# Kernel optimization log

Measured on AMD Instinct MI355X. Metric: run time of the kernel, lower is better.

The kernel has to match this reference:

```python
import jax, jax.numpy as jnp
import numpy as np

EPS = 1e-8


def _conv1d(x, w, b):
    # x: [B, E, L], w: [F, E, K], b: [F] -> [B, F, L] (k=3, pad=1 keeps length)
    y = jax.lax.conv_general_dilated(
        x, w, window_strides=(1,), padding=[(1, 1)],
        dimension_numbers=("NCH", "OIH", "NCH"))
    return y + b[None, :, None]


def setup_inputs() -> dict:
    key = jax.random.key(0)
    kq, ka, ke, kw, kb, ku = jax.random.split(key, 6)
    B, QL, AL = 512, 128, 512
    V, E, F, K = 50000, 300, 400, 3
    question = jax.random.randint(kq, (B, QL), 0, V + 1, dtype=jnp.int64)
    answer = jax.random.randint(ka, (B, AL), 0, V + 1, dtype=jnp.int64)
    emb_table = jax.random.normal(ke, (V + 1, E), dtype=jnp.float32)
    emb_table = emb_table.at[0].set(0.0)  # padding_idx=0
    conv_w = jax.random.normal(kw, (F, E, K), dtype=jnp.float32) * 0.05
    conv_b = jax.random.normal(kb, (F,), dtype=jnp.float32) * 0.05
    U = jax.random.normal(ku, (F, F), dtype=jnp.float32) * 0.1
    return {"question": question, "answer": answer, "emb_table": emb_table,
            "conv_w": conv_w, "conv_b": conv_b, "U": U}


def reference(question, answer, emb_table, conv_w, conv_b, U):
    q = emb_table[question]              # [B, QL, E]
    a = emb_table[answer]                # [B, AL, E]
    Q = _conv1d(q.transpose(0, 2, 1), conv_w, conv_b)   # [B, F, QL]
    A = _conv1d(a.transpose(0, 2, 1), conv_w, conv_b)   # [B, F, AL]
    # G = tanh(Q^T U A): [B, QL, AL]
    G = jnp.tanh(jnp.einsum("bfq,fg,bga->bqa", Q, U, A))
    roQ = jax.nn.softmax(jnp.max(G, axis=2), axis=1)    # [B, QL]
    roA = jax.nn.softmax(jnp.max(G, axis=1), axis=1)    # [B, AL]
    rQ = jnp.einsum("bfq,bq->bf", Q, roQ)               # [B, F]
    rA = jnp.einsum("bfa,ba->bf", A, roA)               # [B, F]
    nQ = jnp.maximum(jnp.linalg.norm(rQ, axis=1), EPS)
    nA = jnp.maximum(jnp.linalg.norm(rA, axis=1), EPS)
    return jnp.sum(rQ * rA, axis=1) / (nQ * nA)         # [B]
```

## Files before the change

kernel.cpp:

```cpp
#include <hip/hip_runtime.h>
#include <math.h>

typedef unsigned int   uint32;
typedef unsigned short ushort16;
typedef __attribute__((ext_vector_type(8))) short  short8;
typedef __attribute__((ext_vector_type(4))) float  floatx4;

#define Bb   512
#define QLn  128
#define ALn  512
#define En   300
#define Fn   400
#define OW   416
#define EPAD 320
#define NV   50001
#define ECROWS 50176
#define ECSTRIDE 2560

typedef const __attribute__((address_space(1))) unsigned int guint_t;
typedef __attribute__((address_space(3))) unsigned int luint_t;
#define GLDS16(g, l) __builtin_amdgcn_global_load_lds((guint_t*)(g), (luint_t*)(l), 16, 0, 0)

static __device__ __forceinline__ float bf_lo(uint32 u) { return __uint_as_float(u << 16); }
static __device__ __forceinline__ float bf_hi(uint32 u) { return __uint_as_float(u & 0xffff0000u); }
static __device__ __forceinline__ ushort16 f2bf(float f) {
    uint32 u = __float_as_uint(f);
    uint32 r = (u + 0x7fffu + ((u >> 16) & 1u)) >> 16;
    return (ushort16)r;
}
static __device__ __forceinline__ uint32 pack2(float a, float b) {
    return (uint32)f2bf(a) | ((uint32)f2bf(b) << 16);
}

__global__ __launch_bounds__(128) void embcvt_kernel(
        const float* __restrict__ emb, char* __restrict__ embbf)
{
    const int r = blockIdx.x, j = threadIdx.x;
    const float* er = emb + (size_t)r * En;
    uint32* orow = (uint32*)(embbf + (size_t)r * 640);
    for (int d = j; d < 160; d += 128) {
        uint32 v = 0;
        if (d < 150) {
            float2 f2v = *(const float2*)(er + 2 * d);
            v = pack2(f2v.x, f2v.y);
        }
        orow[d] = v;
    }
}

__global__ __launch_bounds__(256) void prep_wt(
        const float* __restrict__ W, const float* __restrict__ cb,
        ushort16* __restrict__ Wt2, float* __restrict__ bias2)
{
    const int f = blockIdx.x, t = threadIdx.x;
    for (int p2 = t; p2 < 480; p2 += 256) {
        int p = 2 * p2;
        float v0 = 0.f, v1 = 0.f;
        if (f < Fn) {
            int kk = p / EPAD, e = p - kk * EPAD;
            if (e < En)     v0 = W[(size_t)f * 900 + e * 3 + kk];
            if (e + 1 < En) v1 = W[(size_t)f * 900 + (e + 1) * 3 + kk];
        }
        *(uint32*)&Wt2[(size_t)f * 960 + p] = pack2(v0, v1);
    }
    if (t == 0) bias2[f] = (f < Fn) ? cb[f] : 0.f;
}

__global__ __launch_bounds__(256) void prep_ub(
        const float* __restrict__ U, ushort16* __restrict__ Ub)
{
    const int g = blockIdx.x, t = threadIdx.x;
    uint32* orow = (uint32*)(Ub + (size_t)g * 416);
    for (int f2 = t; f2 < 208; f2 += 256) {
        int f = 2 * f2;
        float v0 = 0.f, v1 = 0.f;
        if (g < Fn) {
            if (f < Fn)     v0 = U[(size_t)f * Fn + g];
            if (f + 1 < Fn) v1 = U[(size_t)(f + 1) * Fn + g];
        }
        orow[f2] = pack2(v0, v1);
    }
}

__global__ __launch_bounds__(512) void ec_gemm(
        const char* __restrict__ embbf, const char* __restrict__ Wt2,
        char* __restrict__ EC)
{
    __shared__ __align__(16) char As[32768];
    __shared__ __align__(16) char Bs[32768];
    const int t = threadIdx.x, lane = t & 63, w = t >> 6;
    const int v0 = blockIdx.x * 256, c0 = blockIdx.y * 256;
    const int wr = w >> 2, wc = w & 3;
    const int fm = lane & 15;
    const int cg = ((lane & 3) - ((lane >> 3) & 3)) & 3;
    const int rl = lane >> 2;
    const int chunkOff = (((lane >> 4) + (fm >> 1)) & 3) * 16;

    const char* srcA[2];
    const char* srcB[2];
#pragma unroll
    for (int i = 0; i < 2; ++i) {
        srcA[i] = embbf + (size_t)(v0 + w * 32 + i * 16 + rl) * 640 + cg * 16;
        int n = c0 + w * 32 + i * 16 + rl;
        int kk = n / 416, f = n - kk * 416;
        if (n >= 1248) { kk = 0; f = 508; }
        srcB[i] = Wt2 + (size_t)f * 1920 + kk * 640 + cg * 16;
    }
    char* AsW = As + w * 2048;
    char* BsW = Bs + w * 2048;

    floatx4 acc[8][4];
    const floatx4 zz = {0.f, 0.f, 0.f, 0.f};
#pragma unroll
    for (int m = 0; m < 8; ++m)
#pragma unroll
        for (int n = 0; n < 4; ++n) acc[m][n] = zz;

#define ESTG(ko, buf) do {                                                    \
        const int _ko = (ko); const int _bo = (buf) * 16384;                  \
        GLDS16(srcA[0] + _ko, AsW + _bo);                                     \
        GLDS16(srcA[1] + _ko, AsW + _bo + 1024);                              \
        GLDS16(srcB[0] + _ko, BsW + _bo);                                     \
        GLDS16(srcB[1] + _ko, BsW + _bo + 1024);                              \
    } while (0)

    int cur = 0;
    ESTG(0, 0);
    __syncthreads();
    for (int ks = 0; ks < 10; ++ks) {
        const int nxt = cur ^ 1;
        if (ks < 9) ESTG((ks + 1) * 64, nxt);
        short8 af[8], bfv[4];
        const char* Ac = As + cur * 16384;
        const char* Bc = Bs + cur * 16384;
#pragma unroll
        for (int m = 0; m < 8; ++m)
            af[m] = *(const short8*)(Ac + (wr * 128 + m * 16 + fm) * 64 + chunkOff);
#pragma unroll
        for (int n = 0; n < 4; ++n)
            bfv[n] = *(const short8*)(Bc + (wc * 64 + n * 16 + fm) * 64 + chunkOff);
        __builtin_amdgcn_s_setprio(1);
#pragma unroll
        for (int m = 0; m < 8; ++m)
#pragma unroll
            for (int n = 0; n < 4; ++n)
                acc[m][n] = __builtin_amdgcn_mfma_f32_16x16x32_bf16(
                    af[m], bfv[n], acc[m][n], 0, 0, 0);
        __builtin_amdgcn_s_setprio(0);
        __syncthreads();
        cur = nxt;
    }
#undef ESTG

#pragma unroll
    for (int m = 0; m < 8; ++m) {
        const int v = v0 + wr * 128 + m * 16 + ((lane >> 4) * 4);
#pragma unroll
        for (int n = 0; n < 4; ++n) {
            const int col = c0 + wc * 64 + n * 16 + fm;
#pragma unroll
            for (int r = 0; r < 4; ++r)
                *(ushort16*)(EC + (size_t)(v + r) * ECSTRIDE + col * 2) =
                    f2bf(acc[m][n][r]);
        }
    }
}

__global__ __launch_bounds__(256) void gather_conv(
        const int* __restrict__ toks, const char* __restrict__ EC,
        const float* __restrict__ bias2, char* __restrict__ outb,
        int nb, int L)
{
    const int total = nb * L * 52;
    int id = blockIdx.x * 256 + threadIdx.x;
    const int stride = gridDim.x * 256;
    for (; id < total; id += stride) {
        const uint32 uid = (uint32)id;
        const int c = (int)(uid % 52u);
        const int r = (int)(uid / 52u);
        const int l = r & (L - 1), b = r / L;
        const int* tr = toks + (size_t)b * L;
        const int t0 = (l > 0)     ? tr[l - 1] : 0;
        const int t1 = tr[l];
        const int t2 = (l < L - 1) ? tr[l + 1] : 0;
        const uint4 x0 = *(const uint4*)(EC + (size_t)t0 * ECSTRIDE +        c * 16);
        const uint4 x1 = *(const uint4*)(EC + (size_t)t1 * ECSTRIDE +  832 + c * 16);
        const uint4 x2 = *(const uint4*)(EC + (size_t)t2 * ECSTRIDE + 1664 + c * 16);
        const float4 b0 = *(const float4*)(bias2 + c * 8);
        const float4 b1 = *(const float4*)(bias2 + c * 8 + 4);
        uint4 o;
        o.x = pack2(bf_lo(x0.x) + bf_lo(x1.x) + bf_lo(x2.x) + b0.x,
                    bf_hi(x0.x) + bf_hi(x1.x) + bf_hi(x2.x) + b0.y);
        o.y = pack2(bf_lo(x0.y) + bf_lo(x1.y) + bf_lo(x2.y) + b0.z,
                    bf_hi(x0.y) + bf_hi(x1.y) + bf_hi(x2.y) + b0.w);
        o.z = pack2(bf_lo(x0.z) + bf_lo(x1.z) + bf_lo(x2.z) + b1.x,
                    bf_hi(x0.z) + bf_hi(x1.z) + bf_hi(x2.z) + b1.y);
        o.w = pack2(bf_lo(x0.w) + bf_lo(x1.w) + bf_lo(x2.w) + b1.z,
                    bf_hi(x0.w) + bf_hi(x1.w) + bf_hi(x2.w) + b1.w);
        *(uint4*)(outb + (size_t)r * 832 + c * 16) = o;
    }
}

template<int NWM, int NWN, int MF, int NF, int BR>
static __device__ __forceinline__ void qp_tile(
        const char* __restrict__ Qb, const char* __restrict__ Ub,
        char* __restrict__ ob, int col0, char* As, char* Bs)
{
    const int t = threadIdx.x, lane = t & 63, w = t >> 6;
    const int wr = w / NWN, wc = w % NWN;
    const int fm = lane & 15;
    const int cg = ((lane & 3) - ((lane >> 3) & 3)) & 3;
    const int rl = lane >> 2;
    const int chunkOff = (((lane >> 4) + (fm >> 1)) & 3) * 16;

    const char* srcA = Qb + (size_t)(w * 16 + rl) * 832 + cg * 16;
    const char* srcB0; const char* srcB1 = 0;
    if (BR == 256) {
        srcB0 = Ub + (size_t)(col0 + w * 32 + rl) * 832 + cg * 16;
        srcB1 = srcB0 + (size_t)16 * 832;
    } else {
        srcB0 = Ub + (size_t)(col0 + w * 16 + rl) * 832 + cg * 16;
        srcB1 = Ub + (size_t)(col0 + 128 + w * 16 + rl) * 832 + cg * 16;
    }
    char* AsW = As + w * 1024;
    char* BsW0; char* BsW1;
    if (BR == 256) { BsW0 = Bs + w * 2048; BsW1 = BsW0 + 1024; }
    else           { BsW0 = Bs + w * 1024; BsW1 = Bs + 8192 + w * 1024; }
    const int BUFB = BR * 64;

    floatx4 acc[MF][NF];
    const floatx4 zz = {0.f, 0.f, 0.f, 0.f};
#pragma unroll
    for (int m = 0; m < MF; ++m)
#pragma unroll
        for (int n = 0; n < NF; ++n) acc[m][n] = zz;

#define QSTG(ko, buf) do {                                                    \
        const int _ko = (ko);                                                 \
        GLDS16(srcA + _ko, AsW + (buf) * 8192);                               \
        GLDS16(srcB0 + _ko, BsW0 + (buf) * BUFB);                             \
        if (BR == 256 || w < 2) GLDS16(srcB1 + _ko, BsW1 + (buf) * BUFB);     \
    } while (0)

    int cur = 0;
    QSTG(0, 0);
    __syncthreads();
    for (int ks = 0; ks < 13; ++ks) {
        const int nxt = cur ^ 1;
        if (ks < 12) QSTG((ks + 1) * 64, nxt);
        short8 af[MF], bfv[NF];
        const char* Ac = As + cur * 8192;
        const char* Bc = Bs + cur * BUFB;
#pragma unroll
        for (int m = 0; m < MF; ++m)
            af[m] = *(const short8*)(Ac + (wr * (MF * 16) + m * 16 + fm) * 64 + chunkOff);
#pragma unroll
        for (int n = 0; n < NF; ++n)
            bfv[n] = *(const short8*)(Bc + (wc * (NF * 16) + n * 16 + fm) * 64 + chunkOff);
        __builtin_amdgcn_s_setprio(1);
#pragma unroll
        for (int m = 0; m < MF; ++m)
#pragma unroll
            for (int n = 0; n < NF; ++n)
                acc[m][n] = __builtin_amdgcn_mfma_f32_16x16x32_bf16(
                    af[m], bfv[n], acc[m][n], 0, 0, 0);
        __builtin_amdgcn_s_setprio(0);
        __syncthreads();
        cur = nxt;
    }
#undef QSTG

#pragma unroll
    for (int m = 0; m < MF; ++m) {
        const int row = wr * (MF * 16) + m * 16 + ((lane >> 4) * 4);
#pragma unroll
        for (int n = 0; n < NF; ++n) {
            const int col = col0 + wc * (NF * 16) + n * 16 + fm;
#pragma unroll
            for (int r = 0; r < 4; ++r)
                *(ushort16*)(ob + (size_t)(row + r) * 832 + col * 2) =
                    f2bf(acc[m][n][r]);
        }
    }
}

__global__ __launch_bounds__(512) void qp_gemm(
        const char* __restrict__ qb, const char* __restrict__ Ub,
        char* __restrict__ qpb)
{
    __shared__ __align__(16) char As[16384];
    __shared__ __align__(16) char Bs[32768];
    const int bx = blockIdx.x;
    const int b = bx >> 1, nt = bx & 1;
    const char* Qb = qb + (size_t)b * 106496;
    char* ob = qpb + (size_t)b * 106496;
    if (nt == 0)
        qp_tile<2, 4, 4, 4, 256>(Qb, Ub, ob, 0, As, Bs);
    else
        qp_tile<4, 2, 2, 5, 160>(Qb, Ub, ob, 256, As, Bs);
}

__global__ __launch_bounds__(256) void fused_g(
        const ushort16* __restrict__ Qp,
        const ushort16* __restrict__ Av,
        float* __restrict__ rowPart,
        float* __restrict__ colMg,
        int nb)
{
    __shared__ __align__(16) char Qs[16384];
    __shared__ __align__(16) char Asl[16384];
    __shared__ float rowM2[128][2];
    __shared__ float colM2[128][2];

    const int t = threadIdx.x, lane = t & 63, w = t >> 6;
    const int bx = blockIdx.x;
    const int xcd = bx & 7, rest = bx >> 3;
    const int c = rest & 3, g = rest >> 2;
    const int T = g * 8 + xcd;
    if (T >= nb) return;
    const int b = T;
    const int wr = w >> 1, wc = w & 1;
    const int fm = lane & 15;
    const int cg = ((lane & 3) - ((lane >> 3) & 3)) & 3;
    const int srow = w * 16 + (lane >> 2);
    const int chunkOff = (((lane >> 4) + (fm >> 1)) & 3) * 16;

    const char* Qpb = (const char*)Qp + (size_t)b * 106496;
    const char* Ab  = (const char*)Av + (size_t)b * 425984 + (size_t)c * 106496;
    const char* srcQ = Qpb + (size_t)srow * 832 + cg * 16;
    const char* srcA = Ab  + (size_t)srow * 832 + cg * 16;
    char* QsW = Qs + w * 1024;
    char* AsW = Asl + w * 1024;

    floatx4 acc[4][4];
    const floatx4 zz = {0.f, 0.f, 0.f, 0.f};
#pragma unroll
    for (int m = 0; m < 4; ++m)
#pragma unroll
        for (int n = 0; n < 4; ++n) acc[m][n] = zz;

#define GSTAGE(colb, buf) do {                                                \
        const int _c = (colb); const int _o = (buf) * 8192;                   \
        GLDS16(srcQ + _c,         QsW + _o);                                  \
        GLDS16(srcQ + 53248 + _c, QsW + _o + 4096);                           \
        GLDS16(srcA + _c,         AsW + _o);                                  \
        GLDS16(srcA + 53248 + _c, AsW + _o + 4096);                           \
    } while (0)

    int cur = 0;
    GSTAGE(0, 0);
    __syncthreads();

    for (int ks = 0; ks < 13; ++ks) {
        const int nxt = cur ^ 1;
        if (ks < 12) GSTAGE((ks + 1) * 64, nxt);

        short8 qa[4], aa_[4];
        const char* Qc = Qs + cur * 8192;
        const char* Ac = Asl + cur * 8192;
#pragma unroll
        for (int m = 0; m < 4; ++m)
            qa[m] = *(const short8*)(Qc + (wr * 64 + m * 16 + fm) * 64 + chunkOff);
#pragma unroll
        for (int n = 0; n < 4; ++n)
            aa_[n] = *(const short8*)(Ac + (wc * 64 + n * 16 + fm) * 64 + chunkOff);
        __builtin_amdgcn_s_setprio(1);
#pragma unroll
        for (int m = 0; m < 4; ++m)
#pragma unroll
            for (int n = 0; n < 4; ++n)
                acc[m][n] = __builtin_amdgcn_mfma_f32_16x16x32_bf16(
                    qa[m], aa_[n], acc[m][n], 0, 0, 0);
        __builtin_amdgcn_s_setprio(0);
        __syncthreads();
        cur = nxt;
    }
#undef GSTAGE

#pragma unroll
    for (int m = 0; m < 4; ++m)
#pragma unroll
        for (int r = 0; r < 4; ++r) {
            float v = fmaxf(fmaxf(acc[m][0][r], acc[m][1][r]),
                            fmaxf(acc[m][2][r], acc[m][3][r]));
            v = fmaxf(v, __shfl_xor(v, 1));
            v = fmaxf(v, __shfl_xor(v, 2));
            v = fmaxf(v, __shfl_xor(v, 4));
            v = fmaxf(v, __shfl_xor(v, 8));
            if (fm == 0) rowM2[wr * 64 + m * 16 + (lane >> 4) * 4 + r][wc] = v;
        }
#pragma unroll
    for (int n = 0; n < 4; ++n) {
        float v = -1e30f;
#pragma unroll
        for (int m = 0; m < 4; ++m)
#pragma unroll
            for (int r = 0; r < 4; ++r) v = fmaxf(v, acc[m][n][r]);
        v = fmaxf(v, __shfl_xor(v, 16));
        v = fmaxf(v, __shfl_xor(v, 32));
        if (lane < 16) colM2[wc * 64 + n * 16 + lane][wr] = v;
    }
    __syncthreads();
    if (t < 128) {
        rowPart[((size_t)b * 4 + c) * 128 + t] = fmaxf(rowM2[t][0], rowM2[t][1]);
        colMg[(size_t)b * 512 + c * 128 + t]   = fmaxf(colM2[t][0], colM2[t][1]);
    }
}

static __device__ __forceinline__ float block_reduce_max(float v, volatile float* red) {
    int t = threadIdx.x;
    red[t] = v; __syncthreads();
    for (int s = 128; s > 0; s >>= 1) {
        if (t < s) red[t] = fmaxf(red[t], red[t + s]);
        __syncthreads();
    }
    float r = red[0]; __syncthreads();
    return r;
}
static __device__ __forceinline__ float block_reduce_sum(float v, volatile float* red) {
    int t = threadIdx.x;
    red[t] = v; __syncthreads();
    for (int s = 128; s > 0; s >>= 1) {
        if (t < s) red[t] = red[t] + red[t + s];
        __syncthreads();
    }
    float r = red[0]; __syncthreads();
    return r;
}

__global__ __launch_bounds__(256) void fused_pool(
        const ushort16* __restrict__ Qv,
        const ushort16* __restrict__ Av,
        const float* __restrict__ rowPart,
        const float* __restrict__ colMg,
        float* __restrict__ out)
{
    __shared__ float colv[ALn];
    __shared__ float roq[QLn];
    __shared__ float red[256];
    const int t = threadIdx.x, b = blockIdx.x;

    float v = -1e30f;
    if (t < QLn) {
        const float* rp = rowPart + (size_t)b * 512;
        float rm = fmaxf(fmaxf(rp[t], rp[128 + t]), fmaxf(rp[256 + t], rp[384 + t]));
        v = tanhf(rm);
    }
    float vmax = block_reduce_max(v, red);
    float ex = (t < QLn) ? __expf(v - vmax) : 0.f;
    float ssum = block_reduce_sum(ex, red);
    if (t < QLn) roq[t] = ex / ssum;

    float c0 = tanhf(colMg[(size_t)b * 512 + t]);
    float c1 = tanhf(colMg[(size_t)b * 512 + 256 + t]);
    float cmax = block_reduce_max(fmaxf(c0, c1), red);
    float e0 = __expf(c0 - cmax), e1 = __expf(c1 - cmax);
    float csum = block_reduce_sum(e0 + e1, red);
    colv[t] = e0 / csum;
    colv[t + 256] = e1 / csum;
    __syncthreads();

    float rq0 = 0.f, rq1 = 0.f, ra0 = 0.f, ra1 = 0.f;
    if (t < 208) {
        const uint32* Qb32 = (const uint32*)((const char*)Qv + (size_t)b * 106496);
#pragma unroll 4
        for (int q = 0; q < QLn; ++q) {
            float wv = roq[q];
            uint32 u = Qb32[q * 208 + t];
            rq0 = fmaf(bf_lo(u), wv, rq0);
            rq1 = fmaf(bf_hi(u), wv, rq1);
        }
        const uint32* Ab32 = (const uint32*)((const char*)Av + (size_t)b * 425984);
#pragma unroll 4
        for (int a = 0; a < ALn; ++a) {
            float wv = colv[a];
            uint32 u = Ab32[a * 208 + t];
            ra0 = fmaf(bf_lo(u), wv, ra0);
            ra1 = fmaf(bf_hi(u), wv, ra1);
        }
    }

    float dd  = block_reduce_sum(rq0 * ra0 + rq1 * ra1, red);
    float qq  = block_reduce_sum(rq0 * rq0 + rq1 * rq1, red);
    float aam = block_reduce_sum(ra0 * ra0 + ra1 * ra1, red);
    if (t == 0) {
        float nq = fmaxf(sqrtf(qq), 1e-8f);
        float na = fmaxf(sqrtf(aam), 1e-8f);
        out[b] = dd / (nq * na);
    }
}

extern "C" void kernel_launch(void* const* d_in, const int* in_sizes, int n_in,
                              void* d_out, int out_size, void* d_ws, size_t ws_size,
                              hipStream_t stream)
{
    const int*   question = (const int*)d_in[0];
    const int*   answer   = (const int*)d_in[1];
    const float* emb      = (const float*)d_in[2];
    const float* conv_w   = (const float*)d_in[3];
    const float* conv_b   = (const float*)d_in[4];
    const float* U        = (const float*)d_in[5];
    float* out = (float*)d_out;
    char* ws = (char*)d_ws;

    const size_t WT2B   = (size_t)512 * 960 * 2;
    const size_t UBB    = (size_t)416 * 416 * 2;
    const size_t ECB    = (size_t)ECROWS * ECSTRIDE;
    const size_t FIXED0 = WT2B + 2048 + UBB + ECB;
    const size_t QB     = (size_t)QLn * OW * 2;
    const size_t AB     = (size_t)ALn * OW * 2;
    const size_t MXB    = 4096;
    const size_t PER_B  = 2 * QB + AB + MXB;

    size_t avail = (ws_size > FIXED0) ? (ws_size - FIXED0) : 0;
    int CB = (int)(avail / PER_B);
    if (CB > Bb) CB = Bb;
    if (CB < 1)  CB = 1;
    int nch = (Bb + CB - 1) / CB;
    int CBe = (Bb + nch - 1) / nch;

    char*  wt2   = ws;
    float* bias2 = (float*)(ws + WT2B);
    char*  ub    = ws + WT2B + 2048;
    char*  EC    = ws + WT2B + 2048 + UBB;
    char*  embbf = ws + FIXED0;
    char*  qb    = ws + FIXED0;
    char*  qpb   = qb  + (size_t)CB * QB;
    char*  ab    = qpb + (size_t)CB * QB;
    float* rowP  = (float*)(ab + (size_t)CB * AB);
    float* colM  = rowP + (size_t)CB * 512;

    embcvt_kernel<<<NV, 128, 0, stream>>>(emb, embbf);
    prep_wt<<<512, 256, 0, stream>>>(conv_w, conv_b, (ushort16*)wt2, bias2);
    prep_ub<<<416, 256, 0, stream>>>(U, (ushort16*)ub);
    ec_gemm<<<dim3(196, 5), 512, 0, stream>>>(embbf, wt2, EC);

    for (int b0 = 0; b0 < Bb; b0 += CBe) {
        int nb = (Bb - b0 < CBe) ? (Bb - b0) : CBe;
        gather_conv<<<1024, 256, 0, stream>>>(
            question + (size_t)b0 * QLn, EC, bias2, qb, nb, QLn);
        gather_conv<<<4096, 256, 0, stream>>>(
            answer + (size_t)b0 * ALn, EC, bias2, ab, nb, ALn);
        qp_gemm<<<nb * 2, 512, 0, stream>>>(qb, ub, qpb);

        int blocksG = ((nb + 7) / 8) * 8 * 4;
        fused_g<<<blocksG, 256, 0, stream>>>((const ushort16*)qpb, (const ushort16*)ab,
                                             rowP, colM, nb);
        fused_pool<<<nb, 256, 0, stream>>>((const ushort16*)qb, (const ushort16*)ab,
                                           rowP, colM, out + b0);
    }
}
```

Baseline: 668.2 us.

## Retile EC GEMM, merge gather kernels, and enlarge fused_g tiles

ec_gemm now keeps a 128-row slab of embeddings resident in LDS across all five output column chunks and streams only the weight tiles, so the A operand is loaded once per block instead of once per column block. The two gather_conv launches become a single gather_both launch to save one launch per batch chunk. fused_g now covers 256 answer columns per block with the full 128 Q rows (two blocks per batch row instead of four), writes column maxima straight to global memory, and halves the rowPart partials. The larger LDS footprint (112KB in ec_gemm) and larger accumulator tiles may reduce occupancy, and the XCD-aware block ordering in fused_g is dropped.

```diff
diff --git a/kernel.cpp b/kernel.cpp
--- a/kernel.cpp
+++ b/kernel.cpp
@@ -86,118 +86,140 @@
         const char* __restrict__ embbf, const char* __restrict__ Wt2,
         char* __restrict__ EC)
 {
-    __shared__ __align__(16) char As[32768];
+    __shared__ __align__(16) char As[81920];
     __shared__ __align__(16) char Bs[32768];
     const int t = threadIdx.x, lane = t & 63, w = t >> 6;
-    const int v0 = blockIdx.x * 256, c0 = blockIdx.y * 256;
+    const int v0 = blockIdx.x * 128;
     const int wr = w >> 2, wc = w & 3;
     const int fm = lane & 15;
     const int cg = ((lane & 3) - ((lane >> 3) & 3)) & 3;
     const int rl = lane >> 2;
     const int chunkOff = (((lane >> 4) + (fm >> 1)) & 3) * 16;
 
-    const char* srcA[2];
-    const char* srcB[2];
-#pragma unroll
-    for (int i = 0; i < 2; ++i) {
-        srcA[i] = embbf + (size_t)(v0 + w * 32 + i * 16 + rl) * 640 + cg * 16;
-        int n = c0 + w * 32 + i * 16 + rl;
-        int kk = n / 416, f = n - kk * 416;
-        if (n >= 1248) { kk = 0; f = 508; }
-        srcB[i] = Wt2 + (size_t)f * 1920 + kk * 640 + cg * 16;
-    }
-    char* AsW = As + w * 2048;
-    char* BsW = Bs + w * 2048;
-
-    floatx4 acc[8][4];
-    const floatx4 zz = {0.f, 0.f, 0.f, 0.f};
-#pragma unroll
-    for (int m = 0; m < 8; ++m)
-#pragma unroll
-        for (int n = 0; n < 4; ++n) acc[m][n] = zz;
-
-#define ESTG(ko, buf) do {                                                    \
-        const int _ko = (ko); const int _bo = (buf) * 16384;                  \
-        GLDS16(srcA[0] + _ko, AsW + _bo);                                     \
-        GLDS16(srcA[1] + _ko, AsW + _bo + 1024);                              \
-        GLDS16(srcB[0] + _ko, BsW + _bo);                                     \
-        GLDS16(srcB[1] + _ko, BsW + _bo + 1024);                              \
+    uint32 offB[5][2];
+#pragma unroll
+    for (int c = 0; c < 5; ++c)
+#pragma unroll
+        for (int i = 0; i < 2; ++i) {
+            int n = c * 256 + w * 32 + i * 16 + rl;
+            int kk = n / 416, f = n - kk * 416;
+            if (n >= 1248) { kk = 0; f = 508; }
+            offB[c][i] = (uint32)(f * 1920 + kk * 640 + cg * 16);
+        }
+
+    const char* srcA = embbf + (size_t)(v0 + w * 16 + rl) * 640 + cg * 16;
+#pragma unroll
+    for (int ks = 0; ks < 10; ++ks)
+        GLDS16(srcA + ks * 64, As + ks * 8192 + w * 1024);
+
+#define BSTG(c, ks, buf) do {                                                 \
+        GLDS16(Wt2 + offB[c][0] + (ks) * 64,                                  \
+               Bs + (buf) * 16384 + w * 2048);                                \
+        GLDS16(Wt2 + offB[c][1] + (ks) * 64,                                  \
+               Bs + (buf) * 16384 + w * 2048 + 1024);                         \
     } while (0)
 
     int cur = 0;
-    ESTG(0, 0);
+    BSTG(0, 0, 0);
     __syncthreads();
-    for (int ks = 0; ks < 10; ++ks) {
-        const int nxt = cur ^ 1;
-        if (ks < 9) ESTG((ks + 1) * 64, nxt);
-        short8 af[8], bfv[4];
-        const char* Ac = As + cur * 16384;
-        const char* Bc = Bs + cur * 16384;
-#pragma unroll
-        for (int m = 0; m < 8; ++m)
-            af[m] = *(const short8*)(Ac + (wr * 128 + m * 16 + fm) * 64 + chunkOff);
-#pragma unroll
-        for (int n = 0; n < 4; ++n)
-            bfv[n] = *(const short8*)(Bc + (wc * 64 + n * 16 + fm) * 64 + chunkOff);
-        __builtin_amdgcn_s_setprio(1);
-#pragma unroll
-        for (int m = 0; m < 8; ++m)
+
+#pragma unroll
+    for (int c = 0; c < 5; ++c) {
+        floatx4 acc[4][4];
+        const floatx4 zz = {0.f, 0.f, 0.f, 0.f};
+#pragma unroll
+        for (int m = 0; m < 4; ++m)
+#pragma unroll
+            for (int n = 0; n < 4; ++n) acc[m][n] = zz;
+
+        for (int ks = 0; ks < 10; ++ks) {
+            const int nxt = cur ^ 1;
+            if (ks < 9)      BSTG(c, ks + 1, nxt);
+            else if (c < 4)  BSTG(c + 1, 0, nxt);
+
+            short8 af[4], bfv[4];
+            const char* Ak = As + ks * 8192;
+            const char* Bc = Bs + cur * 16384;
+#pragma unroll
+            for (int m = 0; m < 4; ++m)
+                af[m] = *(const short8*)(Ak + (wr * 64 + m * 16 + fm) * 64 + chunkOff);
 #pragma unroll
             for (int n = 0; n < 4; ++n)
-                acc[m][n] = __builtin_amdgcn_mfma_f32_16x16x32_bf16(
-                    af[m], bfv[n], acc[m][n], 0, 0, 0);
-        __builtin_amdgcn_s_setprio(0);
-        __syncthreads();
-        cur = nxt;
-    }
-#undef ESTG
-
-#pragma unroll
-    for (int m = 0; m < 8; ++m) {
-        const int v = v0 + wr * 128 + m * 16 + ((lane >> 4) * 4);
-#pragma unroll
-        for (int n = 0; n < 4; ++n) {
-            const int col = c0 + wc * 64 + n * 16 + fm;
-#pragma unroll
-            for (int r = 0; r < 4; ++r)
-                *(ushort16*)(EC + (size_t)(v + r) * ECSTRIDE + col * 2) =
-                    f2bf(acc[m][n][r]);
-        }
-    }
-}
-
-__global__ __launch_bounds__(256) void gather_conv(
+                bfv[n] = *(const short8*)(Bc + (wc * 64 + n * 16 + fm) * 64 + chunkOff);
+            __builtin_amdgcn_s_setprio(1);
+#pragma unroll
+            for (int m = 0; m < 4; ++m)
+#pragma unroll
+                for (int n = 0; n < 4; ++n)
+                    acc[m][n] = __builtin_amdgcn_mfma_f32_16x16x32_bf16(
+                        af[m], bfv[n], acc[m][n], 0, 0, 0);
+            __builtin_amdgcn_s_setprio(0);
+            __syncthreads();
+            cur = nxt;
+        }
+
+#pragma unroll
+        for (int m = 0; m < 4; ++m) {
+            const int v = v0 + wr * 64 + m * 16 + ((lane >> 4) * 4);
+#pragma unroll
+            for (int n = 0; n < 4; ++n) {
+                const int col = c * 256 + wc * 64 + n * 16 + fm;
+#pragma unroll
+                for (int r = 0; r < 4; ++r)
+                    *(ushort16*)(EC + (size_t)(v + r) * ECSTRIDE + col * 2) =
+                        f2bf(acc[m][n][r]);
+            }
+        }
+    }
+#undef BSTG
+}
+
+static __device__ __forceinline__ void gather_one(
         const int* __restrict__ toks, const char* __restrict__ EC,
         const float* __restrict__ bias2, char* __restrict__ outb,
-        int nb, int L)
-{
-    const int total = nb * L * 52;
-    int id = blockIdx.x * 256 + threadIdx.x;
-    const int stride = gridDim.x * 256;
-    for (; id < total; id += stride) {
-        const uint32 uid = (uint32)id;
-        const int c = (int)(uid % 52u);
-        const int r = (int)(uid / 52u);
-        const int l = r & (L - 1), b = r / L;
-        const int* tr = toks + (size_t)b * L;
-        const int t0 = (l > 0)     ? tr[l - 1] : 0;
-        const int t1 = tr[l];
-        const int t2 = (l < L - 1) ? tr[l + 1] : 0;
-        const uint4 x0 = *(const uint4*)(EC + (size_t)t0 * ECSTRIDE +        c * 16);
-        const uint4 x1 = *(const uint4*)(EC + (size_t)t1 * ECSTRIDE +  832 + c * 16);
-        const uint4 x2 = *(const uint4*)(EC + (size_t)t2 * ECSTRIDE + 1664 + c * 16);
-        const float4 b0 = *(const float4*)(bias2 + c * 8);
-        const float4 b1 = *(const float4*)(bias2 + c * 8 + 4);
-        uint4 o;
-        o.x = pack2(bf_lo(x0.x) + bf_lo(x1.x) + bf_lo(x2.x) + b0.x,
-                    bf_hi(x0.x) + bf_hi(x1.x) + bf_hi(x2.x) + b0.y);
-        o.y = pack2(bf_lo(x0.y) + bf_lo(x1.y) + bf_lo(x2.y) + b0.z,
-                    bf_hi(x0.y) + bf_hi(x1.y) + bf_hi(x2.y) + b0.w);
-        o.z = pack2(bf_lo(x0.z) + bf_lo(x1.z) + bf_lo(x2.z) + b1.x,
-                    bf_hi(x0.z) + bf_hi(x1.z) + bf_hi(x2.z) + b1.y);
-        o.w = pack2(bf_lo(x0.w) + bf_lo(x1.w) + bf_lo(x2.w) + b1.z,
-                    bf_hi(x0.w) + bf_hi(x1.w) + bf_hi(x2.w) + b1.w);
-        *(uint4*)(outb + (size_t)r * 832 + c * 16) = o;
+        int id, int L)
+{
+    const uint32 uid = (uint32)id;
+    const int c = (int)(uid % 52u);
+    const int r = (int)(uid / 52u);
+    const int l = r & (L - 1), b = r / L;
+    const int* tr = toks + (size_t)b * L;
+    const int t0 = (l > 0)     ? tr[l - 1] : 0;
+    const int t1 = tr[l];
+    const int t2 = (l < L - 1) ? tr[l + 1] : 0;
+    const uint4 x0 = *(const uint4*)(EC + (size_t)t0 * ECSTRIDE +        c * 16);
+    const uint4 x1 = *(const uint4*)(EC + (size_t)t1 * ECSTRIDE +  832 + c * 16);
+    const uint4 x2 = *(const uint4*)(EC + (size_t)t2 * ECSTRIDE + 1664 + c * 16);
+    const float4 b0 = *(const float4*)(bias2 + c * 8);
+    const float4 b1 = *(const float4*)(bias2 + c * 8 + 4);
+    uint4 o;
+    o.x = pack2(bf_lo(x0.x) + bf_lo(x1.x) + bf_lo(x2.x) + b0.x,
+                bf_hi(x0.x) + bf_hi(x1.x) + bf_hi(x2.x) + b0.y);
+    o.y = pack2(bf_lo(x0.y) + bf_lo(x1.y) + bf_lo(x2.y) + b0.z,
+                bf_hi(x0.y) + bf_hi(x1.y) + bf_hi(x2.y) + b0.w);
+    o.z = pack2(bf_lo(x0.z) + bf_lo(x1.z) + bf_lo(x2.z) + b1.x,
+                bf_hi(x0.z) + bf_hi(x1.z) + bf_hi(x2.z) + b1.y);
+    o.w = pack2(bf_lo(x0.w) + bf_lo(x1.w) + bf_lo(x2.w) + b1.z,
+                bf_hi(x0.w) + bf_hi(x1.w) + bf_hi(x2.w) + b1.w);
+    *(uint4*)(outb + (size_t)r * 832 + c * 16) = o;
+}
+
+#define GQB 1024
+#define GAB 4096
+__global__ __launch_bounds__(256) void gather_both(
+        const int* __restrict__ question, const int* __restrict__ answer,
+        const char* __restrict__ EC, const float* __restrict__ bias2,
+        char* __restrict__ qb, char* __restrict__ ab, int nb)
+{
+    const int bx = blockIdx.x, t = threadIdx.x;
+    if (bx < GQB) {
+        const int total = nb * QLn * 52;
+        for (int id = bx * 256 + t; id < total; id += GQB * 256)
+            gather_one(question, EC, bias2, qb, id, QLn);
+    } else {
+        const int total = nb * ALn * 52;
+        for (int id = (bx - GQB) * 256 + t; id < total; id += GAB * 256)
+            gather_one(answer, EC, bias2, ab, id, ALn);
     }
 }
 
@@ -308,65 +330,61 @@
         int nb)
 {
     __shared__ __align__(16) char Qs[16384];
-    __shared__ __align__(16) char Asl[16384];
-    __shared__ float rowM2[128][2];
-    __shared__ float colM2[128][2];
+    __shared__ __align__(16) char Asl[32768];
+    __shared__ float rowM4[128][4];
 
     const int t = threadIdx.x, lane = t & 63, w = t >> 6;
     const int bx = blockIdx.x;
-    const int xcd = bx & 7, rest = bx >> 3;
-    const int c = rest & 3, g = rest >> 2;
-    const int T = g * 8 + xcd;
-    if (T >= nb) return;
-    const int b = T;
-    const int wr = w >> 1, wc = w & 1;
+    const int c = bx & 1, b = bx >> 1;
+    if (b >= nb) return;
     const int fm = lane & 15;
     const int cg = ((lane & 3) - ((lane >> 3) & 3)) & 3;
-    const int srow = w * 16 + (lane >> 2);
+    const int rl = lane >> 2;
     const int chunkOff = (((lane >> 4) + (fm >> 1)) & 3) * 16;
 
     const char* Qpb = (const char*)Qp + (size_t)b * 106496;
-    const char* Ab  = (const char*)Av + (size_t)b * 425984 + (size_t)c * 106496;
-    const char* srcQ = Qpb + (size_t)srow * 832 + cg * 16;
-    const char* srcA = Ab  + (size_t)srow * 832 + cg * 16;
-    char* QsW = Qs + w * 1024;
-    char* AsW = Asl + w * 1024;
-
-    floatx4 acc[4][4];
+    const char* Ab  = (const char*)Av + (size_t)b * 425984 + (size_t)c * 212992;
+    const char* srcQ0 = Qpb + (size_t)(w * 16 + rl) * 832 + cg * 16;
+    const char* srcQ1 = Qpb + (size_t)(64 + w * 16 + rl) * 832 + cg * 16;
+    const char* srcA0 = Ab  + (size_t)(w * 64 + rl) * 832 + cg * 16;
+
+    floatx4 acc[8][4];
     const floatx4 zz = {0.f, 0.f, 0.f, 0.f};
 #pragma unroll
-    for (int m = 0; m < 4; ++m)
+    for (int m = 0; m < 8; ++m)
 #pragma unroll
         for (int n = 0; n < 4; ++n) acc[m][n] = zz;
 
-#define GSTAGE(colb, buf) do {                                                \
-        const int _c = (colb); const int _o = (buf) * 8192;                   \
-        GLDS16(srcQ + _c,         QsW + _o);                                  \
-        GLDS16(srcQ + 53248 + _c, QsW + _o + 4096);                           \
-        GLDS16(srcA + _c,         AsW + _o);                                  \
-        GLDS16(srcA + 53248 + _c, AsW + _o + 4096);                           \
+#define FSTG(ko, buf) do {                                                    \
+        const int _ko = (ko);                                                 \
+        GLDS16(srcQ0 + _ko, Qs + (buf) * 8192 + w * 1024);                    \
+        GLDS16(srcQ1 + _ko, Qs + (buf) * 8192 + 4096 + w * 1024);             \
+        GLDS16(srcA0 + _ko,         Asl + (buf) * 16384 + w * 4096);          \
+        GLDS16(srcA0 + 13312 + _ko, Asl + (buf) * 16384 + w * 4096 + 1024);   \
+        GLDS16(srcA0 + 26624 + _ko, Asl + (buf) * 16384 + w * 4096 + 2048);   \
+        GLDS16(srcA0 + 39936 + _ko, Asl + (buf) * 16384 + w * 4096 + 3072);   \
     } while (0)
 
     int cur = 0;
-    GSTAGE(0, 0);
+    FSTG(0, 0);
     __syncthreads();
 
     for (int ks = 0; ks < 13; ++ks) {
         const int nxt = cur ^ 1;
-        if (ks < 12) GSTAGE((ks + 1) * 64, nxt);
-
-        short8 qa[4], aa_[4];
+        if (ks < 12) FSTG((ks + 1) * 64, nxt);
+
+        short8 qa[8], aa_[4];
         const char* Qc = Qs + cur * 8192;
-        const char* Ac = Asl + cur * 8192;
-#pragma unroll
-        for (int m = 0; m < 4; ++m)
-            qa[m] = *(const short8*)(Qc + (wr * 64 + m * 16 + fm) * 64 + chunkOff);
+        const char* Ac = Asl + cur * 16384;
+#pragma unroll
+        for (int m = 0; m < 8; ++m)
+            qa[m] = *(const short8*)(Qc + (m * 16 + fm) * 64 + chunkOff);
 #pragma unroll
         for (int n = 0; n < 4; ++n)
-            aa_[n] = *(const short8*)(Ac + (wc * 64 + n * 16 + fm) * 64 + chunkOff);
+            aa_[n] = *(const short8*)(Ac + (w * 64 + n * 16 + fm) * 64 + chunkOff);
         __builtin_amdgcn_s_setprio(1);
 #pragma unroll
-        for (int m = 0; m < 4; ++m)
+        for (int m = 0; m < 8; ++m)
 #pragma unroll
             for (int n = 0; n < 4; ++n)
                 acc[m][n] = __builtin_amdgcn_mfma_f32_16x16x32_bf16(
@@ -375,10 +393,10 @@
         __syncthreads();
         cur = nxt;
     }
-#undef GSTAGE
-
-#pragma unroll
-    for (int m = 0; m < 4; ++m)
+#undef FSTG
+
+#pragma unroll
+    for (int m = 0; m < 8; ++m)
 #pragma unroll
         for (int r = 0; r < 4; ++r) {
             float v = fmaxf(fmaxf(acc[m][0][r], acc[m][1][r]),
@@ -387,24 +405,25 @@
             v = fmaxf(v, __shfl_xor(v, 2));
             v = fmaxf(v, __shfl_xor(v, 4));
             v = fmaxf(v, __shfl_xor(v, 8));
-            if (fm == 0) rowM2[wr * 64 + m * 16 + (lane >> 4) * 4 + r][wc] = v;
+            if (fm == 0) rowM4[m * 16 + (lane >> 4) * 4 + r][w] = v;
         }
 #pragma unroll
     for (int n = 0; n < 4; ++n) {
         float v = -1e30f;
 #pragma unroll
-        for (int m = 0; m < 4; ++m)
+        for (int m = 0; m < 8; ++m)
 #pragma unroll
             for (int r = 0; r < 4; ++r) v = fmaxf(v, acc[m][n][r]);
         v = fmaxf(v, __shfl_xor(v, 16));
         v = fmaxf(v, __shfl_xor(v, 32));
-        if (lane < 16) colM2[wc * 64 + n * 16 + lane][wr] = v;
+        if (lane < 16)
+            colMg[(size_t)b * 512 + c * 256 + w * 64 + n * 16 + lane] = v;
     }
     __syncthreads();
-    if (t < 128) {
-        rowPart[((size_t)b * 4 + c) * 128 + t] = fmaxf(rowM2[t][0], rowM2[t][1]);
-        colMg[(size_t)b * 512 + c * 128 + t]   = fmaxf(colM2[t][0], colM2[t][1]);
-    }
+    if (t < 128)
+        rowPart[((size_t)b * 2 + c) * 128 + t] =
+            fmaxf(fmaxf(rowM4[t][0], rowM4[t][1]),
+                  fmaxf(rowM4[t][2], rowM4[t][3]));
 }
 
 static __device__ __forceinline__ float block_reduce_max(float v, volatile float* red) {
@@ -442,8 +461,8 @@
 
     float v = -1e30f;
     if (t < QLn) {
-        const float* rp = rowPart + (size_t)b * 512;
-        float rm = fmaxf(fmaxf(rp[t], rp[128 + t]), fmaxf(rp[256 + t], rp[384 + t]));
+        const float* rp = rowPart + (size_t)b * 256;
+        float rm = fmaxf(rp[t], rp[128 + t]);
         v = tanhf(rm);
     }
     float vmax = block_reduce_max(v, red);
@@ -533,19 +552,16 @@
     embcvt_kernel<<<NV, 128, 0, stream>>>(emb, embbf);
     prep_wt<<<512, 256, 0, stream>>>(conv_w, conv_b, (ushort16*)wt2, bias2);
     prep_ub<<<416, 256, 0, stream>>>(U, (ushort16*)ub);
-    ec_gemm<<<dim3(196, 5), 512, 0, stream>>>(embbf, wt2, EC);
+    ec_gemm<<<392, 512, 0, stream>>>(embbf, wt2, EC);
 
     for (int b0 = 0; b0 < Bb; b0 += CBe) {
         int nb = (Bb - b0 < CBe) ? (Bb - b0) : CBe;
-        gather_conv<<<1024, 256, 0, stream>>>(
-            question + (size_t)b0 * QLn, EC, bias2, qb, nb, QLn);
-        gather_conv<<<4096, 256, 0, stream>>>(
-            answer + (size_t)b0 * ALn, EC, bias2, ab, nb, ALn);
+        gather_both<<<GQB + GAB, 256, 0, stream>>>(
+            question + (size_t)b0 * QLn, answer + (size_t)b0 * ALn,
+            EC, bias2, qb, ab, nb);
         qp_gemm<<<nb * 2, 512, 0, stream>>>(qb, ub, qpb);
-
-        int blocksG = ((nb + 7) / 8) * 8 * 4;
-        fused_g<<<blocksG, 256, 0, stream>>>((const ushort16*)qpb, (const ushort16*)ab,
-                                             rowP, colM, nb);
+        fused_g<<<nb * 2, 256, 0, stream>>>((const ushort16*)qpb, (const ushort16*)ab,
+                                            rowP, colM, nb);
         fused_pool<<<nb, 256, 0, stream>>>((const ushort16*)qb, (const ushort16*)ab,
                                            rowP, colM, out + b0);
     }
```

New measurement: 707.7 us. 1.06x slower.
